# Kernel optimization log

Hardware: AMD Instinct MI355X
Metric: run time of the kernel (lower is better)

Reference implementation:

```python
import jax, jax.numpy as jnp
import numpy as np
import math

B, T, D = 4, 2048, 1024
N, D_OUT = 1024, 1024
EPS_A = 1e-4
PROJ_BOUND = 1.0


def setup_inputs() -> dict:
    key = jax.random.key(0)
    ks = jax.random.split(key, 4)
    # reset_parameters: rho=0.99, delta0=1.0
    rho, delta0 = 0.99, 1.0
    alpha0 = -math.log(rho) / delta0
    alpha_log_val = math.log(math.expm1(alpha0))
    delta_bias_val = math.log(math.expm1(delta0))
    return {
        "u": jax.random.normal(ks[0], (B, T, D), dtype=jnp.float32),
        "z0": jnp.zeros((B, N), dtype=jnp.float32),
        "W_in_raw": 0.02 * jax.random.normal(ks[1], (N, D), dtype=jnp.float32),
        "W_out_raw": 0.02 * jax.random.normal(ks[2], (D_OUT, N), dtype=jnp.float32),
        "pn_w": 0.02 * jax.random.normal(ks[3], (3 * N, D), dtype=jnp.float32),
        "pn_b": jnp.zeros((3 * N,), dtype=jnp.float32),
        "alpha_log": jnp.full((N,), alpha_log_val, dtype=jnp.float32),
        "delta_bias": jnp.full((N,), delta_bias_val, dtype=jnp.float32),
        "log_gamma": jnp.float32(0.0),
    }


def _bounded_linear(x, W, bound):
    # y = x @ (W/scale)^T with ||W/scale||_2 <= bound (exact spectral norm)
    sigma = jnp.maximum(jnp.linalg.norm(W, ord=2), 1e-5)
    scale = jnp.maximum(sigma / bound, 1.0)
    return x @ (W / scale).T


def reference(u, z0, W_in_raw, W_out_raw, pn_w, pn_b, alpha_log, delta_bias, log_gamma):
    g = jnp.exp(log_gamma)
    u_scaled = g * _bounded_linear(u, W_in_raw, PROJ_BOUND)        # (B,T,N)
    raw = u @ pn_w.T + pn_b                                        # (B,T,3N)
    delta_raw, b_raw, c_raw = jnp.split(raw, 3, axis=-1)
    delta = jax.nn.softplus(delta_raw + delta_bias)
    alpha = jax.nn.softplus(alpha_log)                             # (N,)
    a = jnp.minimum(jnp.exp(-delta * alpha), 1.0 - EPS_A)          # (B,T,N)
    b = jnp.tanh(b_raw)
    c = jnp.tanh(c_raw)
    # exact spectral norm of [[a,b],[c,0]] per coordinate
    p = a * a + c * c
    r = b * b
    q = a * b
    disc = (p - r) * (p - r) + 4.0 * q * q
    lam_max = 0.5 * (p + r + jnp.sqrt(disc + 1e-12))
    sigma = jnp.sqrt(lam_max + 1e-12)
    scale = jnp.maximum(sigma, 1.0)
    a, b, c = a / scale, b / scale, c / scale
    # diagonal recurrence z_{t+1} = a_t * z_t + b_t * u_scaled_t via associative scan
    bu = b * u_scaled
    bu = bu.at[:, 0].add(a[:, 0] * z0)
    def combine(x, y):
        a1, b1 = x
        a2, b2 = y
        return (a2 * a1, a2 * b1 + b2)
    _, z_next = jax.lax.associative_scan(combine, (a, bu), axis=1)  # z_1..z_T (B,T,N)
    # y_t = W_out (c_t * z_t) with z_t = state BEFORE update (one-step delay)
    states = jnp.concatenate([z0[:, None, :], z_next[:, :-1, :]], axis=1)  # z_0..z_{T-1}
    y_hat = c * states
    y = _bounded_linear(y_hat, W_out_raw, PROJ_BOUND)              # (B,T,D_out)
    return y
```

## Files before the change

kernel.cpp:

```cpp
#include <hip/hip_runtime.h>
#include <stdint.h>

#define B_ 4
#define T_ 2048
#define D_ 1024
#define N_ 1024
#define TC 16
#define NCH (T_/TC)
#define SQN 6

typedef __attribute__((ext_vector_type(4))) float f32x4;
typedef __attribute__((ext_vector_type(8))) short bf16x8;
typedef __attribute__((ext_vector_type(4))) unsigned short us4;

__device__ __forceinline__ unsigned short f2bf(float f){
  unsigned int u = __float_as_uint(f);
  return (unsigned short)((u + 0x7fffu + ((u >> 16) & 1u)) >> 16);
}
__device__ __forceinline__ float bf2f(unsigned short h){
  return __uint_as_float(((unsigned int)h) << 16);
}

__device__ __forceinline__ float inv_scale(const float* __restrict__ sc, int z){
  float ll = 0.f, w = 1.f, t = 1.f;
  #pragma unroll
  for (int i = 0; i <= SQN; i++){
    t = sc[8 + 2*i + z];
    ll += w * __logf(t);
    w *= 0.5f;
  }
  float F = sc[8 + 2*(SQN+1) + z];
  ll += w * __logf(F / (t*t));
  float sig = fmaxf(__expf(0.5f * ll), 1e-5f);
  return 1.f / fmaxf(sig, 1.f);
}

__device__ __forceinline__ float softplusf(float x){
  return (x > 0.f) ? (x + __logf(1.f + __expf(-x))) : __logf(1.f + __expf(x));
}
__device__ __forceinline__ float tanhfastf(float x){
  float e = __expf(2.f * x);
  return 1.f - 2.f/(e + 1.f);
}

#define U4    2097152
#define WIN4   262144
#define PNW4   786432
#define WOUT4  262144
#define CONV_BLOCKS ((U4 + WIN4 + PNW4 + WOUT4 + 255)/256)

__global__ void k_convert_all(const float* __restrict__ u, const float* __restrict__ Win,
                              const float* __restrict__ pnw, const float* __restrict__ Wout,
                              unsigned short* __restrict__ u16, unsigned short* __restrict__ Wcat16,
                              unsigned short* __restrict__ Wout16, float* __restrict__ sc){
  if (blockIdx.x == 0 && threadIdx.x < 64) sc[threadIdx.x] = 0.f;
  long i = (long)blockIdx.x * 256 + threadIdx.x;
  const float* src; long o; size_t didx; unsigned short* dbuf;
  if (i < U4){
    src = u; o = i; dbuf = u16; didx = (size_t)o;
  } else if (i < U4+WIN4){
    o = i - U4; src = Win;
    int n = (int)(o >> 8), c4 = (int)(o & 255);
    dbuf = Wcat16; didx = (size_t)(4*n)*256 + c4;
  } else if (i < U4+WIN4+PNW4){
    o = i - (U4+WIN4); src = pnw;
    int m = (int)(o >> 8), c4 = (int)(o & 255);
    int s = (m >> 10) + 1, n = m & 1023;
    dbuf = Wcat16; didx = (size_t)(4*n + s)*256 + c4;
  } else if (i < U4+WIN4+PNW4+WOUT4){
    o = i - (U4+WIN4+PNW4); src = Wout; dbuf = Wout16; didx = (size_t)o;
  } else return;
  float4 v = ((const float4*)src)[o];
  us4 w;
  w.x = f2bf(v.x); w.y = f2bf(v.y); w.z = f2bf(v.z); w.w = f2bf(v.w);
  ((us4*)dbuf)[didx] = w;
}

__device__ __forceinline__ void load_lds16(const unsigned short* g, unsigned short* l){
  __builtin_amdgcn_global_load_lds((const __attribute__((address_space(1))) void*)g,
                                   (__attribute__((address_space(3))) void*)l, 16, 0, 0);
}

__global__ __launch_bounds__(256) void k_pgemm(
    const unsigned short* __restrict__ A,
    const unsigned short* __restrict__ Bmat,
    const float* __restrict__ alog, const float* __restrict__ dbias,
    const float* __restrict__ pnb, const float* __restrict__ lgam,
    const float* __restrict__ sc,
    unsigned int* __restrict__ G1,
    float* __restrict__ G2)
{
  __shared__ alignas(16) char smem[36864];
  unsigned short* As = (unsigned short*)smem;
  unsigned short* Bs = (unsigned short*)(smem + 16384);
  const int tid = threadIdx.x;
  const int wid = tid >> 6;
  const int lane = tid & 63;
  const int bn = blockIdx.x, bm = blockIdx.y;
  const int K = 1024;

  const int wr = wid >> 1, wc = wid & 1;
  const int rg = lane >> 3;
  const int cby = (lane & 7) << 4;
  const int srow0 = wid * 32;
  const int frow = lane & 15;
  const int kgrp = lane >> 4;

  const unsigned short* ap[4];
  const unsigned short* bp[4];
  unsigned short* adst[4];
  unsigned short* bdst[4];
  #pragma unroll
  for (int i = 0; i < 4; i++){
    int r = srow0 + i*8 + rg;
    int cb = cby ^ ((r & 7) << 4);
    ap[i] = A    + (size_t)(bm*128 + r)*K + (cb >> 1);
    bp[i] = Bmat + (size_t)(bn*128 + r)*K + (cb >> 1);
    adst[i] = As + (srow0 + i*8)*64;
    bdst[i] = Bs + (srow0 + i*8)*64;
  }
  int aoff[4][2], boff[4][2];
  #pragma unroll
  for (int m = 0; m < 4; m++){
    int r = wr*64 + m*16 + frow;
    #pragma unroll
    for (int kk = 0; kk < 2; kk++)
      aoff[m][kk] = r*128 + ((kk*64 + kgrp*16) ^ ((r & 7) << 4));
  }
  #pragma unroll
  for (int n2 = 0; n2 < 4; n2++){
    int r = wc*64 + n2*16 + frow;
    #pragma unroll
    for (int kk = 0; kk < 2; kk++)
      boff[n2][kk] = r*128 + ((kk*64 + kgrp*16) ^ ((r & 7) << 4));
  }

  f32x4 acc[4][4] = {};

  for (int kt = 0; kt < K; kt += 64){
    #pragma unroll
    for (int i = 0; i < 4; i++){
      load_lds16(ap[i], adst[i]);
      load_lds16(bp[i], bdst[i]);
      ap[i] += 64; bp[i] += 64;
    }
    __syncthreads();
    #pragma unroll
    for (int kk = 0; kk < 2; kk++){
      bf16x8 af[4], bfv[4];
      #pragma unroll
      for (int m = 0; m < 4; m++)
        af[m] = *(const bf16x8*)((const char*)As + aoff[m][kk]);
      #pragma unroll
      for (int n2 = 0; n2 < 4; n2++)
        bfv[n2] = *(const bf16x8*)((const char*)Bs + boff[n2][kk]);
      #pragma unroll
      for (int m = 0; m < 4; m++)
        #pragma unroll
        for (int n2 = 0; n2 < 4; n2++)
          acc[m][n2] = __builtin_amdgcn_mfma_f32_16x16x32_bf16(bfv[n2], af[m], acc[m][n2], 0, 0, 0);
    }
    __syncthreads();
  }

  unsigned int* g1s = (unsigned int*)smem;
  float*        g2s = (float*)(smem + 18432);

  const float ginv = __expf(lgam[0]) * inv_scale(sc, 0);
  float alpha[4], bd[4], bb[4], bc[4];
  #pragma unroll
  for (int nw = 0; nw < 4; nw++){
    int n = bn*32 + wc*16 + nw*4 + kgrp;
    alpha[nw] = softplusf(alog[n]);
    bd[nw] = dbias[n] + pnb[n];
    bb[nw] = pnb[N_ + n];
    bc[nw] = pnb[2*N_ + n];
  }
  #pragma unroll
  for (int mu = 0; mu < 4; mu++){
    const int tl = wr*64 + mu*16 + frow;
    #pragma unroll
    for (int nw = 0; nw < 4; nw++){
      const int nl = wc*16 + nw*4 + kgrp;
      f32x4 v = acc[mu][nw];
      float lp = __logf(1.f + __expf(v[1] + bd[nw]));
      float av = fminf(__expf(-alpha[nw]*lp), 1.f - 1e-4f);
      float bv = tanhfastf(v[2] + bb[nw]);
      float cv = tanhfastf(v[3] + bc[nw]);
      float p = av*av + cv*cv;
      float r = bv*bv;
      float q = av*bv;
      float pr = p - r;
      float disc = pr*pr + 4.f*q*q;
      float lam = 0.5f*(p + r + sqrtf(disc + 1e-12f));
      float inv = fminf(rsqrtf(lam + 1e-12f), 1.f);
      float a = av * inv;
      float c = cv * inv;
      float bu = (bv * inv) * (v[0] * ginv);
      g1s[tl*36 + nl] = (unsigned int)f2bf(a) | ((unsigned int)f2bf(c) << 16);
      g2s[tl*36 + nl] = bu;
    }
  }
  __syncthreads();
  const size_t t0b = (size_t)bm * 128;
  const int nb = bn*32;
  #pragma unroll
  for (int r = 0; r < 4; r++){
    int flat = r*256 + tid;
    int tl = flat >> 3, seg = flat & 7;
    uint4  v1 = *(const uint4*)(g1s + tl*36 + seg*4);
    float4 v2 = *(const float4*)(g2s + tl*36 + seg*4);
    *(uint4*)(G1 + (t0b + tl)*N_ + nb + seg*4) = v1;
    *(float4*)(G2 + (t0b + tl)*N_ + nb + seg*4) = v2;
  }
}

template<int OUTBF16>
__global__ __launch_bounds__(256) void k_gemm(
    const unsigned short* __restrict__ A,
    const unsigned short* __restrict__ Bmat,
    void* __restrict__ C0,
    int M, int N, int K,
    const float* __restrict__ sc, int step)
{
  __shared__ alignas(16) unsigned short As[128*64];
  __shared__ alignas(16) unsigned short Bs[128*64];
  const int tid = threadIdx.x;
  const int wid = tid >> 6;
  const int lane = tid & 63;
  const int bn = blockIdx.x, bm = blockIdx.y;

  char* C = (char*)C0;
  float outscale = (step >= 0) ? inv_scale(sc, step) : 1.f;

  const int wr = wid >> 1, wc = wid & 1;
  const int rg = lane >> 3;
  const int cby = (lane & 7) << 4;
  const int srow0 = wid * 32;
  const int frow = lane & 15;
  const int kgrp = lane >> 4;

  const unsigned short* ap[4];
  const unsigned short* bp[4];
  unsigned short* adst[4];
  unsigned short* bdst[4];
  #pragma unroll
  for (int i = 0; i < 4; i++){
    int r = srow0 + i*8 + rg;
    int cb = cby ^ ((r & 7) << 4);
    ap[i] = A    + (size_t)(bm*128 + r)*K + (cb >> 1);
    bp[i] = Bmat + (size_t)(bn*128 + r)*K + (cb >> 1);
    adst[i] = As + (srow0 + i*8)*64;
    bdst[i] = Bs + (srow0 + i*8)*64;
  }
  int aoff[4][2], boff[4][2];
  #pragma unroll
  for (int m = 0; m < 4; m++){
    int r = wr*64 + m*16 + frow;
    #pragma unroll
    for (int kk = 0; kk < 2; kk++)
      aoff[m][kk] = r*128 + ((kk*64 + kgrp*16) ^ ((r & 7) << 4));
  }
  #pragma unroll
  for (int n2 = 0; n2 < 4; n2++){
    int r = wc*64 + n2*16 + frow;
    #pragma unroll
    for (int kk = 0; kk < 2; kk++)
      boff[n2][kk] = r*128 + ((kk*64 + kgrp*16) ^ ((r & 7) << 4));
  }

  f32x4 acc[4][4] = {};

  for (int kt = 0; kt < K; kt += 64){
    #pragma unroll
    for (int i = 0; i < 4; i++){
      load_lds16(ap[i], adst[i]);
      load_lds16(bp[i], bdst[i]);
      ap[i] += 64; bp[i] += 64;
    }
    __syncthreads();
    #pragma unroll
    for (int kk = 0; kk < 2; kk++){
      bf16x8 af[4], bfv[4];
      #pragma unroll
      for (int m = 0; m < 4; m++)
        af[m] = *(const bf16x8*)((const char*)As + aoff[m][kk]);
      #pragma unroll
      for (int n2 = 0; n2 < 4; n2++)
        bfv[n2] = *(const bf16x8*)((const char*)Bs + boff[n2][kk]);
      #pragma unroll
      for (int m = 0; m < 4; m++)
        #pragma unroll
        for (int n2 = 0; n2 < 4; n2++)
          acc[m][n2] = __builtin_amdgcn_mfma_f32_16x16x32_bf16(af[m], bfv[n2], acc[m][n2], 0, 0, 0);
    }
    __syncthreads();
  }

  const int row0 = bm*128 + wr*64;
  const int col0 = bn*128 + wc*64 + frow;
  #pragma unroll
  for (int m = 0; m < 4; m++){
    #pragma unroll
    for (int n2 = 0; n2 < 4; n2++){
      const int col = col0 + n2*16;
      const int rb = row0 + m*16 + kgrp*4;
      #pragma unroll
      for (int j = 0; j < 4; j++){
        float v = acc[m][n2][j] * outscale;
        if (OUTBF16) ((unsigned short*)C)[(size_t)(rb + j)*N + col] = f2bf(v);
        else         ((float*)C)[(size_t)(rb + j)*N + col] = v;
      }
    }
  }
}

__global__ __launch_bounds__(256) void k_sq(
    const unsigned short* __restrict__ A0, unsigned short* __restrict__ C0,
    const unsigned short* __restrict__ A1, unsigned short* __restrict__ C1,
    float* __restrict__ sc, int step)
{
  __shared__ alignas(16) unsigned short As0[64*128], Bs0[64*128];
  __shared__ alignas(16) unsigned short As1[64*128], Bs1[64*128];
  const int tid = threadIdx.x;
  const int wid = tid >> 6;
  const int lane = tid & 63;
  const int z = blockIdx.z;

  int x = blockIdx.x, bm = 0;
  while (x >= 16 - bm){ x -= 16 - bm; bm++; }
  const int bn = bm + x;

  const unsigned short* A = z ? A1 : A0;
  unsigned short* C = z ? C1 : C0;
  const size_t rs = (step == 0 && z == 0) ? 4096 : 1024;
  float outscale = 1.f;
  if (step > 0){ float t = sc[8 + (step-1)*2 + z]; outscale = 1.f/(t*t); }

  const int wr = wid >> 1, wc = wid & 1;
  const int frow = lane & 15;
  const int kgrp = lane >> 4;

  const int srl = lane >> 4;
  const int sgr = lane & 15;
  const int swzr = wid*4 + srl;
  const int scol_e = ((sgr ^ swzr) << 3);

  const size_t Arow = (size_t)bm * 64;
  const size_t Brow = (size_t)bn * 64;

  f32x4 acc[2][2] = {};

  auto stage = [&](unsigned short* as, unsigned short* bs, int t){
    const int kt = t * 128;
    #pragma unroll
    for (int i = 0; i < 4; i++){
      int r = i*16 + wid*4 + srl;
      load_lds16(A + (Arow + r)*rs + kt + scol_e, as + (i*16 + wid*4)*128);
      load_lds16(A + (Brow + r)*rs + kt + scol_e, bs + (i*16 + wid*4)*128);
    }
  };

  auto compute = [&](const unsigned short* as, const unsigned short* bs){
    #pragma unroll
    for (int ks = 0; ks < 4; ks++){
      const int kb = ks*64 + kgrp*16;
      bf16x8 af[2], bfv[2];
      #pragma unroll
      for (int m = 0; m < 2; m++){
        int r = wr*32 + m*16 + frow;
        af[m] = *(const bf16x8*)((const char*)as + r*256 + (kb ^ (frow << 4)));
      }
      #pragma unroll
      for (int n2 = 0; n2 < 2; n2++){
        int r = wc*32 + n2*16 + frow;
        bfv[n2] = *(const bf16x8*)((const char*)bs + r*256 + (kb ^ (frow << 4)));
      }
      #pragma unroll
      for (int m = 0; m < 2; m++)
        #pragma unroll
        for (int n2 = 0; n2 < 2; n2++)
          acc[m][n2] = __builtin_amdgcn_mfma_f32_16x16x32_bf16(af[m], bfv[n2], acc[m][n2], 0, 0, 0);
    }
  };

  stage(As0, Bs0, 0);
  __syncthreads();
  for (int t2 = 0; t2 < 8; t2 += 2){
    if (t2 + 1 < 8) stage(As1, Bs1, t2 + 1);
    compute(As0, Bs0);
    __syncthreads();
    if (t2 + 2 < 8) stage(As0, Bs0, t2 + 2);
    compute(As1, Bs1);
    __syncthreads();
  }

  const int row0 = bm*64 + wr*32;
  const int col0 = bn*64 + wc*32 + frow;
  float fr = 0.f;
  #pragma unroll
  for (int m = 0; m < 2; m++){
    #pragma unroll
    for (int n2 = 0; n2 < 2; n2++){
      const int col = col0 + n2*16;
      const int rb = row0 + m*16 + kgrp*4;
      us4 tw;
      #pragma unroll
      for (int j = 0; j < 4; j++){
        float v = acc[m][n2][j] * outscale;
        unsigned short h = f2bf(v);
        C[(size_t)(rb + j)*1024 + col] = h;
        tw[j] = h;
        fr += v*v;
      }
      if (bm != bn)
        *(us4*)(C + (size_t)col*1024 + rb) = tw;
    }
  }
  if (bm == bn && wr == wc){
    int j = frow - kgrp*4;
    if (j >= 0 && j < 4){
      float d = (acc[0][0][j] + acc[1][1][j]) * outscale;
      atomicAdd(&sc[8 + step*2 + z], d);
    }
  }
  if (step == SQN){
    if (bm != bn) fr *= 2.f;
    #pragma unroll
    for (int off = 32; off; off >>= 1) fr += __shfl_down(fr, off, 64);
    if (lane == 0) atomicAdd(&sc[8 + 2*(SQN+1) + z], fr);
  }
}

__global__ __launch_bounds__(256) void k_scanA(
    const unsigned int* __restrict__ G1, const float* __restrict__ G2,
    float* __restrict__ Asum, float* __restrict__ Ssum)
{
  const int tid = threadIdx.x;
  const int n0 = blockIdx.y*512 + tid*2;
  const int ch = blockIdx.x, b = blockIdx.z;
  const size_t base = (size_t)(b*T_ + ch*TC)*N_ + n0;

  uint2 g1[TC]; float2 g2[TC];
  #pragma unroll
  for (int i = 0; i < TC; i++){
    g1[i] = *(const uint2*)(G1 + base + (size_t)i*N_);
    g2[i] = *(const float2*)(G2 + base + (size_t)i*N_);
  }
  float A0 = 1.f, A1 = 1.f, S0 = 0.f, S1 = 0.f;
  #pragma unroll
  for (int i = 0; i < TC; i++){
    float a0 = bf2f((unsigned short)(g1[i].x & 0xffffu));
    float a1 = bf2f((unsigned short)(g1[i].y & 0xffffu));
    S0 = fmaf(a0, S0, g2[i].x); A0 *= a0;
    S1 = fmaf(a1, S1, g2[i].y); A1 *= a1;
  }
  const size_t idx = (size_t)(b*NCH + ch)*N_ + n0;
  *(float2*)(Asum + idx) = make_float2(A0, A1);
  *(float2*)(Ssum + idx) = make_float2(S0, S1);
}

__global__ __launch_bounds__(256) void k_scanB(
    const unsigned int* __restrict__ G1, const float* __restrict__ G2,
    const float* __restrict__ Asum, const float* __restrict__ Ssum,
    const float* __restrict__ z0, unsigned short* __restrict__ yh)
{
  const int tid = threadIdx.x;
  const int n0 = tid*4;
  const int ch = blockIdx.x, b = blockIdx.y;
  float z[4];
  #pragma unroll
  for (int j = 0; j < 4; j++) z[j] = z0[b*N_ + n0 + j];
  for (int c2 = 0; c2 < ch; c2++){
    const size_t idx = (size_t)(b*NCH + c2)*N_ + n0;
    float4 Av = *(const float4*)(Asum + idx);
    float4 Sv = *(const float4*)(Ssum + idx);
    z[0] = fmaf(Av.x, z[0], Sv.x);
    z[1] = fmaf(Av.y, z[1], Sv.y);
    z[2] = fmaf(Av.z, z[2], Sv.z);
    z[3] = fmaf(Av.w, z[3], Sv.w);
  }
  const size_t base = (size_t)(b*T_ + ch*TC)*N_ + n0;
  const unsigned int* g1 = G1 + base;
  const float* g2 = G2 + base;
  unsigned short* Y = yh + base;
  #pragma unroll 4
  for (int i = 0; i < TC; i++){
    uint4 pac = *(const uint4*)g1;
    float4 bu = *(const float4*)g2;
    us4 ow;
    #pragma unroll
    for (int j = 0; j < 4; j++){
      unsigned int p = j==0 ? pac.x : j==1 ? pac.y : j==2 ? pac.z : pac.w;
      float buj     = j==0 ? bu.x  : j==1 ? bu.y  : j==2 ? bu.z  : bu.w;
      float a = bf2f((unsigned short)(p & 0xffffu));
      float c = bf2f((unsigned short)(p >> 16));
      float yv = c * z[j];
      z[j] = fmaf(a, z[j], buj);
      ow[j] = f2bf(yv);
    }
    *(us4*)Y = ow;
    g1 += N_; g2 += N_; Y += N_;
  }
}

extern "C" void kernel_launch(void* const* d_in, const int* in_sizes, int n_in,
                              void* d_out, int out_size, void* d_ws, size_t ws_size,
                              hipStream_t stream)
{
  const float* u    = (const float*)d_in[0];
  const float* z0   = (const float*)d_in[1];
  const float* Win  = (const float*)d_in[2];
  const float* Wout = (const float*)d_in[3];
  const float* pnw  = (const float*)d_in[4];
  const float* pnb  = (const float*)d_in[5];
  const float* alog = (const float*)d_in[6];
  const float* dbias= (const float*)d_in[7];
  const float* lgam = (const float*)d_in[8];

  char* ws = (char*)d_ws;
  size_t off = 0;
  auto alloc = [&](size_t bytes) -> void* {
    void* p = ws + off;
    off += (bytes + 255) & ~(size_t)255;
    return p;
  };
  float*          sc     = (float*)         alloc(1024);
  unsigned short* u16    = (unsigned short*)alloc((size_t)8192*1024*2);
  unsigned short* Wcat16 = (unsigned short*)alloc((size_t)4096*1024*2);
  unsigned short* Wout16 = (unsigned short*)alloc((size_t)1024*1024*2);
  unsigned int*   G1     = (unsigned int*)  alloc((size_t)8192*1024*4);
  float*          G2     = (float*)         alloc((size_t)8192*1024*4);
  unsigned short* yh16   = (unsigned short*)alloc((size_t)8192*1024*2);
  unsigned short* Hping  = (unsigned short*)alloc((size_t)2*1024*1024*2);
  unsigned short* Hpong  = (unsigned short*)alloc((size_t)2*1024*1024*2);
  float*          Asum   = (float*)alloc((size_t)B_*NCH*N_*4);
  float*          Ssum   = (float*)alloc((size_t)B_*NCH*N_*4);

  k_convert_all<<<CONV_BLOCKS, 256, 0, stream>>>(u, Win, pnw, Wout, u16, Wcat16, Wout16, sc);

  dim3 gsq(136, 1, 2);
  k_sq<<<gsq, 256, 0, stream>>>(Wcat16, Hping, Wout16, Hping + (size_t)1024*1024, sc, 0);
  unsigned short* hin = Hping;
  unsigned short* hout = Hpong;
  for (int s = 1; s <= SQN; s++){
    k_sq<<<gsq, 256, 0, stream>>>(hin, hout, hin + (size_t)1024*1024, hout + (size_t)1024*1024, sc, s);
    unsigned short* t = hin; hin = hout; hout = t;
  }

  dim3 g1(4096/128, 8192/128);
  k_pgemm<<<g1, 256, 0, stream>>>(u16, Wcat16, alog, dbias, pnb, lgam, sc, G1, G2);

  dim3 ga(NCH, 2, B_);
  k_scanA<<<ga, 256, 0, stream>>>(G1, G2, Asum, Ssum);
  dim3 gb(NCH, B_);
  k_scanB<<<gb, 256, 0, stream>>>(G1, G2, Asum, Ssum, z0, yh16);

  dim3 g2(1024/128, 8192/128);
  k_gemm<0><<<g2, 256, 0, stream>>>(yh16, Wout16, d_out, 8192, 1024, 1024, sc, 1);
}
```

Baseline: 277.6 us.

## Fuse chunk-level scan reduction into projection GEMM epilogue, drop scanA kernel

The per-chunk products and partial sums (Asum/Ssum) are now computed from the LDS-staged epilogue tiles inside the projection GEMM, so the separate scanA kernel and its re-read of G1/G2 from global memory go away. Each 128-row tile covers 8 chunks of 16 timesteps and 32 columns, and one thread handles one chunk and column. The tanh epilogue also swaps division for a hardware reciprocal, which slightly reduces accuracy. The cost is extra serial work and LDS reads at the end of each GEMM block.

```diff
diff --git a/kernel.cpp b/kernel.cpp
--- a/kernel.cpp
+++ b/kernel.cpp
@@ -41,6 +41,10 @@
 __device__ __forceinline__ float tanhfastf(float x){
   float e = __expf(2.f * x);
   return 1.f - 2.f/(e + 1.f);
+}
+__device__ __forceinline__ float tanhrcpf(float x){
+  float e = __expf(2.f * x);
+  return 1.f - 2.f*__builtin_amdgcn_rcpf(e + 1.f);
 }
 
 #define U4    2097152
@@ -88,7 +92,8 @@
     const float* __restrict__ pnb, const float* __restrict__ lgam,
     const float* __restrict__ sc,
     unsigned int* __restrict__ G1,
-    float* __restrict__ G2)
+    float* __restrict__ G2,
+    float* __restrict__ Asum, float* __restrict__ Ssum)
 {
   __shared__ alignas(16) char smem[36864];
   unsigned short* As = (unsigned short*)smem;
@@ -185,8 +190,8 @@
       f32x4 v = acc[mu][nw];
       float lp = __logf(1.f + __expf(v[1] + bd[nw]));
       float av = fminf(__expf(-alpha[nw]*lp), 1.f - 1e-4f);
-      float bv = tanhfastf(v[2] + bb[nw]);
-      float cv = tanhfastf(v[3] + bc[nw]);
+      float bv = tanhrcpf(v[2] + bb[nw]);
+      float cv = tanhrcpf(v[3] + bc[nw]);
       float p = av*av + cv*cv;
       float r = bv*bv;
       float q = av*bv;
@@ -212,6 +217,22 @@
     float4 v2 = *(const float4*)(g2s + tl*36 + seg*4);
     *(uint4*)(G1 + (t0b + tl)*N_ + nb + seg*4) = v1;
     *(float4*)(G2 + (t0b + tl)*N_ + nb + seg*4) = v2;
+  }
+  {
+    const int chl = tid >> 5;
+    const int nl  = tid & 31;
+    float Ar = 1.f, Sr = 0.f;
+    #pragma unroll
+    for (int i = 0; i < 16; i++){
+      int row = chl*16 + i;
+      float a = bf2f((unsigned short)(g1s[row*36 + nl] & 0xffffu));
+      float bu = g2s[row*36 + nl];
+      Sr = fmaf(a, Sr, bu);
+      Ar *= a;
+    }
+    const size_t gch = (size_t)bm*8 + chl;
+    Asum[gch*N_ + nb + nl] = Ar;
+    Ssum[gch*N_ + nb + nl] = Sr;
   }
 }
 
@@ -430,34 +451,6 @@
     for (int off = 32; off; off >>= 1) fr += __shfl_down(fr, off, 64);
     if (lane == 0) atomicAdd(&sc[8 + 2*(SQN+1) + z], fr);
   }
-}
-
-__global__ __launch_bounds__(256) void k_scanA(
-    const unsigned int* __restrict__ G1, const float* __restrict__ G2,
-    float* __restrict__ Asum, float* __restrict__ Ssum)
-{
-  const int tid = threadIdx.x;
-  const int n0 = blockIdx.y*512 + tid*2;
-  const int ch = blockIdx.x, b = blockIdx.z;
-  const size_t base = (size_t)(b*T_ + ch*TC)*N_ + n0;
-
-  uint2 g1[TC]; float2 g2[TC];
-  #pragma unroll
-  for (int i = 0; i < TC; i++){
-    g1[i] = *(const uint2*)(G1 + base + (size_t)i*N_);
-    g2[i] = *(const float2*)(G2 + base + (size_t)i*N_);
-  }
-  float A0 = 1.f, A1 = 1.f, S0 = 0.f, S1 = 0.f;
-  #pragma unroll
-  for (int i = 0; i < TC; i++){
-    float a0 = bf2f((unsigned short)(g1[i].x & 0xffffu));
-    float a1 = bf2f((unsigned short)(g1[i].y & 0xffffu));
-    S0 = fmaf(a0, S0, g2[i].x); A0 *= a0;
-    S1 = fmaf(a1, S1, g2[i].y); A1 *= a1;
-  }
-  const size_t idx = (size_t)(b*NCH + ch)*N_ + n0;
-  *(float2*)(Asum + idx) = make_float2(A0, A1);
-  *(float2*)(Ssum + idx) = make_float2(S0, S1);
 }
 
 __global__ __launch_bounds__(256) void k_scanB(
@@ -549,10 +542,8 @@
   }
 
   dim3 g1(4096/128, 8192/128);
-  k_pgemm<<<g1, 256, 0, stream>>>(u16, Wcat16, alog, dbias, pnb, lgam, sc, G1, G2);
-
-  dim3 ga(NCH, 2, B_);
-  k_scanA<<<ga, 256, 0, stream>>>(G1, G2, Asum, Ssum);
+  k_pgemm<<<g1, 256, 0, stream>>>(u16, Wcat16, alog, dbias, pnb, lgam, sc, G1, G2, Asum, Ssum);
+
   dim3 gb(NCH, B_);
   k_scanB<<<gb, 256, 0, stream>>>(G1, G2, Asum, Ssum, z0, yh16);
 
```

After: 264.4 us. 4.8% less time.
